# Kernel optimization log

Hardware: AMD Instinct MI355X
Metric: run time of the kernel (lower is better)

The kernel has to match this reference:

```python
import math
import jax, jax.numpy as jnp
import numpy as np

L, D, H, DFF, T, B, BUCKETS = 4, 512, 8, 2048, 256, 8, 32
DH = D // H


def _ln(x, g, b, eps=1e-6):
    m = x.mean(-1, keepdims=True)
    v = ((x - m) ** 2).mean(-1, keepdims=True)
    return (x - m) / jnp.sqrt(v + eps) * g + b


def setup_inputs() -> dict:
    key = jax.random.key(0)
    ki = iter(jax.random.split(key, 32))
    p = lambda shape: jax.random.normal(next(ki), shape, jnp.float32) * 0.02
    inp = {}
    inp['src'] = jax.random.normal(next(ki), (T, B, D), jnp.float32)
    inp['lengths'] = jax.random.randint(next(ki), (B,), 128, T + 1)
    inp['distances'] = jax.random.randint(next(ki), (B, T, T), 0, BUCKETS + 1)
    inp['u'] = jax.random.normal(next(ki), (D,), jnp.float32)
    inp['v'] = jax.random.normal(next(ki), (D,), jnp.float32)
    inp['ln1_g'] = jnp.ones((L, D)); inp['ln1_b'] = jnp.zeros((L, D))
    for nm in ['Wq', 'Wk', 'Wv', 'Wo']:
        inp[nm] = p((L, D, D))
    for nm in ['bq', 'bk', 'bv', 'bo']:
        inp[nm] = jnp.zeros((L, D))
    # learned relative-position embedding table per layer, padding row zeroed
    inp['rel_table'] = p((L, BUCKETS + 1, D)).at[:, BUCKETS, :].set(0.0)
    inp['ffn_ln_g'] = jnp.ones((L, D)); inp['ffn_ln_b'] = jnp.zeros((L, D))
    inp['W1'] = p((L, DFF, D)); inp['b1'] = jnp.zeros((L, DFF))
    inp['W2'] = p((L, D, DFF)); inp['b2'] = jnp.zeros((L, D))
    inp['final_ln_g'] = jnp.ones((D,)); inp['final_ln_b'] = jnp.zeros((D,))
    return inp


def reference(src, lengths, distances, u, v, ln1_g, ln1_b, Wq, bq, Wk, bk, Wv, bv,
              Wo, bo, rel_table, ffn_ln_g, ffn_ln_b, W1, b1, W2, b2,
              final_ln_g, final_ln_b):
    # onmt-style sinusoidal positional encoding with sqrt(d_model) scaling
    pos = jnp.arange(T, dtype=jnp.float32)[:, None]
    div = jnp.exp(jnp.arange(0, D, 2, dtype=jnp.float32) * (-math.log(10000.0) / D))
    pe = jnp.zeros((T, D)).at[:, 0::2].set(jnp.sin(pos * div)).at[:, 1::2].set(jnp.cos(pos * div))
    x = (src * math.sqrt(D) + pe[:, None, :]).transpose(1, 0, 2)  # (B,T,D)
    pad = jnp.arange(T)[None, :] >= lengths[:, None]  # (B,T), True = masked key
    uh = u.reshape(1, H, 1, DH)
    vh = v.reshape(1, H, 1, DH)
    for l in range(L):
        h = _ln(x, ln1_g[l], ln1_b[l])
        def heads(w, b_):
            return (h @ w.T + b_).reshape(B, T, H, DH).transpose(0, 2, 1, 3)
        q = heads(Wq[l], bq[l]) / math.sqrt(DH)  # (B,H,T,DH)
        k = heads(Wk[l], bk[l])
        val = heads(Wv[l], bv[l])
        # content term a_c = (q + u) k^T
        a_c = jnp.einsum('bhqd,bhkd->bhqk', q + uh, k)
        # relative term b_d = (q + v) R^T, R gathered per (query,key) pair
        rel = rel_table[l][distances].reshape(B, T, T, H, DH)  # (B,Q,K,H,DH)
        b_d = jnp.einsum('bhqd,bqkhd->bhqk', q + vh, rel)
        scores = (a_c + b_d).astype(jnp.float32)
        scores = jnp.where(pad[:, None, None, :], -1e18, scores)
        attn = jax.nn.softmax(scores, axis=-1)
        ctx = jnp.einsum('bhqk,bhkd->bhqd', attn, val)
        ctx = ctx.transpose(0, 2, 1, 3).reshape(B, T, D)
        out = ctx @ Wo[l].T + bo[l] + x  # residual (dropout=0)
        # PositionwiseFeedForward: LN -> W1 -> relu -> W2 -> +residual
        h2 = _ln(out, ffn_ln_g[l], ffn_ln_b[l])
        x = jax.nn.relu(h2 @ W1[l].T + b1[l]) @ W2[l].T + b2[l] + out
    x = _ln(x, final_ln_g, final_ln_b)
    return x.transpose(1, 0, 2)  # (T,B,D)
```

## Files before the change

kernel.cpp:

```cpp
#include <hip/hip_runtime.h>
#include <hip/hip_bf16.h>
#include <math.h>

constexpr int L = 4, D = 512, H = 8, DFF = 2048, T = 256, B = 8, BUCKETS = 32;
constexpr int DH = D / H;
constexpr int NT = B * T;
constexpr int QKVLD = 3 * D;

typedef __attribute__((ext_vector_type(8))) short bf16x8;
typedef __attribute__((ext_vector_type(4))) float f32x4;

__device__ __forceinline__ unsigned short f2bf(float f) {
    unsigned int x = __float_as_uint(f);
    return (unsigned short)((x + 0x7fffu + ((x >> 16) & 1u)) >> 16);
}
__device__ __forceinline__ float bf2f(unsigned short u) {
    return __uint_as_float((unsigned int)u << 16);
}

__device__ __forceinline__ void stage16(const unsigned short* g, short* l) {
    __builtin_amdgcn_global_load_lds((const __attribute__((address_space(1))) unsigned int*)g,
                                     (__attribute__((address_space(3))) unsigned int*)l,
                                     16, 0, 0);
}

__global__ __launch_bounds__(256) void embed_kernel(const float* __restrict__ src,
                                                    float* __restrict__ x)
{
    int idx = blockIdx.x * 256 + threadIdx.x;
    int d = idx & (D - 1);
    int t = (idx >> 9) & (T - 1);
    int b = idx >> 17;
    int i = d >> 1;
    float div = expf(-(float)(2 * i) * (9.210340371976184f / (float)D));
    float ang = (float)t * div;
    float pe = (d & 1) ? cosf(ang) : sinf(ang);
    x[idx] = src[((size_t)t * B + b) * D + d] * 22.62741699796952f + pe;
}

__device__ __forceinline__ void ln_core(const float* __restrict__ xr,
                                        const float* __restrict__ g,
                                        const float* __restrict__ bb,
                                        float* o0, float* o1, int tid)
{
    float v0 = xr[tid], v1 = xr[tid + 256];
    float s = v0 + v1, q2 = v0 * v0 + v1 * v1;
#pragma unroll
    for (int o = 32; o; o >>= 1) { s += __shfl_xor(s, o); q2 += __shfl_xor(q2, o); }
    __shared__ float rs[4], rq[4];
    int lane = tid & 63, wid = tid >> 6;
    if (lane == 0) { rs[wid] = s; rq[wid] = q2; }
    __syncthreads();
    s = rs[0] + rs[1] + rs[2] + rs[3];
    q2 = rq[0] + rq[1] + rq[2] + rq[3];
    float mean = s * (1.f / (float)D);
    float var = q2 * (1.f / (float)D) - mean * mean;
    float rstd = rsqrtf(var + 1e-6f);
    *o0 = (v0 - mean) * rstd * g[tid] + bb[tid];
    *o1 = (v1 - mean) * rstd * g[tid + 256] + bb[tid + 256];
}

__global__ __launch_bounds__(256) void ln_kernel(const float* __restrict__ x,
                                                 unsigned short* __restrict__ y,
                                                 const float* __restrict__ g,
                                                 const float* __restrict__ bb)
{
    int row = blockIdx.x, tid = threadIdx.x;
    float o0, o1;
    ln_core(x + (size_t)row * D, g, bb, &o0, &o1, tid);
    y[(size_t)row * D + tid] = f2bf(o0);
    y[(size_t)row * D + tid + 256] = f2bf(o1);
}

__global__ __launch_bounds__(256) void final_ln_kernel(const float* __restrict__ x,
                                                       float* __restrict__ out,
                                                       const float* __restrict__ g,
                                                       const float* __restrict__ bb)
{
    int row = blockIdx.x, tid = threadIdx.x;
    int b = row >> 8, t = row & (T - 1);
    float o0, o1;
    ln_core(x + (size_t)row * D, g, bb, &o0, &o1, tid);
    float* op = out + ((size_t)t * B + b) * D;
    op[tid] = o0;
    op[tid + 256] = o1;
}

__global__ __launch_bounds__(256) void convert_layer_kernel(
    const float* __restrict__ Wq, const float* __restrict__ Wk, const float* __restrict__ Wv,
    const float* __restrict__ Wo, const float* __restrict__ W1, const float* __restrict__ W2,
    const float* __restrict__ bq, const float* __restrict__ bk, const float* __restrict__ bv,
    const float* __restrict__ rel, int l,
    unsigned short* __restrict__ WQKVb, unsigned short* __restrict__ Wob,
    unsigned short* __restrict__ W1b, unsigned short* __restrict__ W2b,
    unsigned short* __restrict__ relb,
    float* __restrict__ bqkv)
{
    int g = blockIdx.x * 256 + threadIdx.x;
    const float* src; unsigned short* dst;
    bool zero = false;
    if (g < 98304) {
        int e = g * 8; int piece = e >> 18; int rem = e & 262143;
        src = (piece == 0 ? Wq : piece == 1 ? Wk : Wv) + (size_t)l * 262144 + rem;
        dst = WQKVb + e;
    } else if (g < 131072) {
        int e = (g - 98304) * 8;
        src = Wo + (size_t)l * 262144 + e; dst = Wob + e;
    } else if (g < 262144) {
        int e = (g - 131072) * 8;
        src = W1 + (size_t)l * 1048576 + e; dst = W1b + e;
    } else if (g < 393216) {
        int e = (g - 262144) * 8;
        src = W2 + (size_t)l * 1048576 + e; dst = W2b + e;
    } else {
        int e = (g - 393216) * 8;
        int row = e >> 9, cc = e & 511;
        dst = relb + e;
        if (row < BUCKETS + 1) src = rel + ((size_t)l * (BUCKETS + 1) + row) * 512 + cc;
        else { src = nullptr; zero = true; }
    }
    uint4 o;
    if (zero) { o.x = o.y = o.z = o.w = 0u; }
    else {
        float4 x = *(const float4*)src, y = *(const float4*)(src + 4);
        o.x = (unsigned)f2bf(x.x) | ((unsigned)f2bf(x.y) << 16);
        o.y = (unsigned)f2bf(x.z) | ((unsigned)f2bf(x.w) << 16);
        o.z = (unsigned)f2bf(y.x) | ((unsigned)f2bf(y.y) << 16);
        o.w = (unsigned)f2bf(y.z) | ((unsigned)f2bf(y.w) << 16);
    }
    *(uint4*)dst = o;
    if (g < 3 * D) {
        int piece = g >> 9, r2 = g & 511;
        bqkv[g] = (piece == 0 ? bq : piece == 1 ? bk : bv)[l * 512 + r2];
    }
}

template <bool RELU, bool RESID, bool OUTBF16>
__global__ __launch_bounds__(256) void mgemm_kernel(
    const unsigned short* __restrict__ A,
    const unsigned short* __restrict__ W,
    const float* __restrict__ bias,
    const float* __restrict__ resid,
    void* __restrict__ Cv,
    int N, int M, int K)
{
    __shared__ short smA[2][128 * 32];
    __shared__ short smB[2][128 * 32];
    int tid = threadIdx.x;
    int bn = blockIdx.y * 128;
    int bm = blockIdx.x * 128;
    const unsigned short* Ab = A + (size_t)bn * K;
    const unsigned short* Wb = W + (size_t)bm * K;

    f32x4 acc[4][4];
#pragma unroll
    for (int i = 0; i < 4; i++)
#pragma unroll
        for (int j = 0; j < 4; j++) acc[i][j] = (f32x4){0.f, 0.f, 0.f, 0.f};

    const int c0 = tid, c1 = tid + 256;
    const int r0 = c0 >> 2, p0 = c0 & 3, l0 = p0 ^ ((r0 >> 1) & 3);
    const int r1 = c1 >> 2, p1 = c1 & 3, l1 = p1 ^ ((r1 >> 1) & 3);

    auto stage = [&](int buf, int k0) {
        stage16(Ab + (size_t)r0 * K + k0 + l0 * 8, &smA[buf][c0 * 8]);
        stage16(Ab + (size_t)r1 * K + k0 + l1 * 8, &smA[buf][c1 * 8]);
        stage16(Wb + (size_t)r0 * K + k0 + l0 * 8, &smB[buf][c0 * 8]);
        stage16(Wb + (size_t)r1 * K + k0 + l1 * 8, &smB[buf][c1 * 8]);
    };

    const int lane = tid & 63;
    const int wv = tid >> 6, wr = wv >> 1, wc = wv & 1;
    int aoff[4], boff[4];
#pragma unroll
    for (int i = 0; i < 4; i++) {
        int ra = wr * 64 + i * 16 + (lane & 15);
        int ca = (lane >> 4) ^ ((ra >> 1) & 3);
        aoff[i] = ra * 32 + ca * 8;
        int rb = wc * 64 + i * 16 + (lane & 15);
        int cb = (lane >> 4) ^ ((rb >> 1) & 3);
        boff[i] = rb * 32 + cb * 8;
    }

    stage(0, 0);
    const int nkt = K >> 5;
    for (int kt = 0; kt < nkt; ++kt) {
        __syncthreads();
        int cur = kt & 1;
        if (kt + 1 < nkt) stage(cur ^ 1, (kt + 1) << 5);
        const short* sa = smA[cur];
        const short* sb = smB[cur];
        bf16x8 af[4], bfr[4];
#pragma unroll
        for (int i = 0; i < 4; i++) af[i] = *(const bf16x8*)(sa + aoff[i]);
#pragma unroll
        for (int j = 0; j < 4; j++) bfr[j] = *(const bf16x8*)(sb + boff[j]);
#pragma unroll
        for (int i = 0; i < 4; i++)
#pragma unroll
            for (int j = 0; j < 4; j++)
                acc[i][j] = __builtin_amdgcn_mfma_f32_16x16x32_bf16(af[i], bfr[j], acc[i][j], 0, 0, 0);
    }

#pragma unroll
    for (int j = 0; j < 4; j++) {
        int col = bm + wc * 64 + j * 16 + (lane & 15);
        float bval = bias[col];
#pragma unroll
        for (int i = 0; i < 4; i++) {
            f32x4 v = acc[i][j];
#pragma unroll
            for (int r = 0; r < 4; r++) {
                int row = bn + wr * 64 + i * 16 + (lane >> 4) * 4 + r;
                float val = v[r] + bval;
                if (RELU) val = fmaxf(val, 0.f);
                if (RESID) val += resid[(size_t)row * M + col];
                if (OUTBF16) ((unsigned short*)Cv)[(size_t)row * M + col] = f2bf(val);
                else         ((float*)Cv)[(size_t)row * M + col] = val;
            }
        }
    }
}

__global__ __launch_bounds__(256) void vtrans_kernel(const unsigned short* __restrict__ qkv,
                                                     unsigned short* __restrict__ vt)
{
    __shared__ unsigned short tile[64 * 66];
    int bh = blockIdx.x, b = bh >> 3, h = bh & 7;
    int kc = blockIdx.y * 64;
    int tid = threadIdx.x;
    int r = tid >> 2, c0 = (tid & 3) * 16;
    const unsigned short* rp = qkv + (size_t)(b * T + kc + r) * QKVLD + 2 * D + h * 64 + c0;
    uint4 w0 = *(const uint4*)rp;
    uint4 w1 = *(const uint4*)(rp + 8);
    unsigned short* tp = &tile[r * 66 + c0];
    unsigned int ww[8] = {w0.x, w0.y, w0.z, w0.w, w1.x, w1.y, w1.z, w1.w};
#pragma unroll
    for (int e = 0; e < 8; e++) {
        tp[2 * e]     = (unsigned short)(ww[e] & 0xffffu);
        tp[2 * e + 1] = (unsigned short)(ww[e] >> 16);
    }
    __syncthreads();
    int d = tid >> 2, k0 = (tid & 3) * 16;
    unsigned int outw[8];
#pragma unroll
    for (int i = 0; i < 8; i++) {
        unsigned int lo = tile[(k0 + 2 * i) * 66 + d];
        unsigned int hi = tile[(k0 + 2 * i + 1) * 66 + d];
        outw[i] = lo | (hi << 16);
    }
    unsigned short* op = vt + (size_t)(bh * 64 + d) * 256 + kc + k0;
    *(uint4*)op = *(uint4*)&outw[0];
    *(uint4*)(op + 8) = *(uint4*)&outw[4];
}

__global__ __launch_bounds__(256) void fattn_kernel(
    const unsigned short* __restrict__ qkv,
    const unsigned short* __restrict__ vt,
    const unsigned short* __restrict__ relb,
    const float* __restrict__ uvec,
    const float* __restrict__ vvec,
    const int* __restrict__ dist,
    const int* __restrict__ lengths,
    unsigned short* __restrict__ ctx)
{
    __shared__ unsigned short Ps[4][16][256];
    __shared__ float Qrel[4][16][49];

    int bh = blockIdx.x, b = bh >> 3, h = bh & 7;
    int qi0 = blockIdx.y * 64;
    int tid = threadIdx.x, w = tid >> 6, lane = tid & 63;
    int l15 = lane & 15, g = lane >> 4;
    int qr = qi0 + w * 16;

    const unsigned short* qbase = qkv + (size_t)(b * T + qr + l15) * QKVLD + h * 64 + g * 8;
    bf16x8 qa0 = *(const bf16x8*)(qbase);
    bf16x8 qa1 = *(const bf16x8*)(qbase + 32);

    bf16x8 qu0, qu1;
    {
        const float* up = uvec + h * 64 + g * 8;
        float ua0[8], ua1[8];
        *(float4*)&ua0[0] = *(const float4*)(up);
        *(float4*)&ua0[4] = *(const float4*)(up + 4);
        *(float4*)&ua1[0] = *(const float4*)(up + 32);
        *(float4*)&ua1[4] = *(const float4*)(up + 36);
#pragma unroll
        for (int e = 0; e < 8; e++) {
            qu0[e] = (short)f2bf(0.125f * bf2f((unsigned short)qa0[e]) + ua0[e]);
            qu1[e] = (short)f2bf(0.125f * bf2f((unsigned short)qa1[e]) + ua1[e]);
        }
    }

    {
        const float* vp = vvec + h * 64 + g * 8;
        float va0[8], va1[8];
        *(float4*)&va0[0] = *(const float4*)(vp);
        *(float4*)&va0[4] = *(const float4*)(vp + 4);
        *(float4*)&va1[0] = *(const float4*)(vp + 32);
        *(float4*)&va1[4] = *(const float4*)(vp + 36);
        bf16x8 qh0, qh1;
#pragma unroll
        for (int e = 0; e < 8; e++) {
            qh0[e] = (short)f2bf(0.125f * bf2f((unsigned short)qa0[e]) + va0[e]);
            qh1[e] = (short)f2bf(0.125f * bf2f((unsigned short)qa1[e]) + va1[e]);
        }
        f32x4 qacc[3];
#pragma unroll
        for (int j = 0; j < 3; j++) qacc[j] = (f32x4){0.f, 0.f, 0.f, 0.f};
#pragma unroll
        for (int j = 0; j < 3; j++) {
            const unsigned short* rp = relb + (size_t)(j * 16 + l15) * 512 + h * 64 + g * 8;
            bf16x8 r0 = *(const bf16x8*)(rp);
            bf16x8 r1 = *(const bf16x8*)(rp + 32);
            qacc[j] = __builtin_amdgcn_mfma_f32_16x16x32_bf16(qh0, r0, qacc[j], 0, 0, 0);
            qacc[j] = __builtin_amdgcn_mfma_f32_16x16x32_bf16(qh1, r1, qacc[j], 0, 0, 0);
        }
#pragma unroll
        for (int j = 0; j < 3; j++)
#pragma unroll
            for (int r = 0; r < 4; r++)
                Qrel[w][g * 4 + r][j * 16 + l15] = qacc[j][r];
    }

    f32x4 acc[16];
#pragma unroll
    for (int j = 0; j < 16; j++) acc[j] = (f32x4){0.f, 0.f, 0.f, 0.f};
    const unsigned short* kbase = qkv + (size_t)(b * T) * QKVLD + 512 + h * 64 + g * 8;
#pragma unroll
    for (int j = 0; j < 16; j++) {
        const unsigned short* kp = kbase + (size_t)(j * 16 + l15) * QKVLD;
        bf16x8 k0 = *(const bf16x8*)(kp);
        bf16x8 k1 = *(const bf16x8*)(kp + 32);
        acc[j] = __builtin_amdgcn_mfma_f32_16x16x32_bf16(qu0, k0, acc[j], 0, 0, 0);
        acc[j] = __builtin_amdgcn_mfma_f32_16x16x32_bf16(qu1, k1, acc[j], 0, 0, 0);
    }

    int len = lengths[b];
    float rinv[4];
    const int* db = dist + (size_t)b * T * T;
#pragma unroll
    for (int r = 0; r < 4; r++) {
        int rowloc = g * 4 + r;
        int qrow = qr + rowloc;
        const int* dpr = db + (size_t)qrow * T;
        float m = -3.0e38f;
#pragma unroll
        for (int j = 0; j < 16; j++) {
            int ki = j * 16 + l15;
            int dv = dpr[ki];
            float s = acc[j][r] + Qrel[w][rowloc][dv];
            s = (ki < len) ? s : -1.0e30f;
            acc[j][r] = s;
            m = fmaxf(m, s);
        }
#pragma unroll
        for (int o = 8; o; o >>= 1) m = fmaxf(m, __shfl_xor(m, o));
        float sum = 0.f;
#pragma unroll
        for (int j = 0; j < 16; j++) {
            int ki = j * 16 + l15;
            float p = __expf(acc[j][r] - m);
            sum += p;
            int cph = ((ki >> 3) ^ (rowloc & 7));
            Ps[w][rowloc][cph * 8 + (ki & 7)] = f2bf(p);
        }
#pragma unroll
        for (int o = 8; o; o >>= 1) sum += __shfl_xor(sum, o);
        rinv[r] = 1.0f / sum;
    }

    f32x4 oacc[4];
#pragma unroll
    for (int j = 0; j < 4; j++) oacc[j] = (f32x4){0.f, 0.f, 0.f, 0.f};
    const unsigned short* vtb = vt + (size_t)bh * 64 * 256;
#pragma unroll
    for (int ks = 0; ks < 8; ks++) {
        int c = ks * 4 + g;
        int cph = c ^ (l15 & 7);
        bf16x8 pa = *(const bf16x8*)&Ps[w][l15][cph * 8];
#pragma unroll
        for (int j2 = 0; j2 < 4; j2++) {
            bf16x8 vb = *(const bf16x8*)(vtb + (size_t)(j2 * 16 + l15) * 256 + c * 8);
            oacc[j2] = __builtin_amdgcn_mfma_f32_16x16x32_bf16(pa, vb, oacc[j2], 0, 0, 0);
        }
    }

#pragma unroll
    for (int j2 = 0; j2 < 4; j2++) {
#pragma unroll
        for (int r = 0; r < 4; r++) {
            int qrow = qr + g * 4 + r;
            int dcol = j2 * 16 + l15;
            ctx[(size_t)(b * T + qrow) * D + h * 64 + dcol] = f2bf(oacc[j2][r] * rinv[r]);
        }
    }
}

extern "C" void kernel_launch(void* const* d_in, const int* in_sizes, int n_in,
                              void* d_out, int out_size, void* d_ws, size_t ws_size,
                              hipStream_t stream)
{
    const float* src     = (const float*)d_in[0];
    const int*   lengths = (const int*)d_in[1];
    const int*   dist    = (const int*)d_in[2];
    const float* u       = (const float*)d_in[3];
    const float* v       = (const float*)d_in[4];
    const float* ln1_g   = (const float*)d_in[5];
    const float* ln1_b   = (const float*)d_in[6];
    const float* Wq      = (const float*)d_in[7];
    const float* Wk      = (const float*)d_in[8];
    const float* Wv      = (const float*)d_in[9];
    const float* Wo      = (const float*)d_in[10];
    const float* bq      = (const float*)d_in[11];
    const float* bk      = (const float*)d_in[12];
    const float* bv      = (const float*)d_in[13];
    const float* bo      = (const float*)d_in[14];
    const float* rel     = (const float*)d_in[15];
    const float* fg      = (const float*)d_in[16];
    const float* fb      = (const float*)d_in[17];
    const float* W1      = (const float*)d_in[18];
    const float* b1      = (const float*)d_in[19];
    const float* W2      = (const float*)d_in[20];
    const float* b2      = (const float*)d_in[21];
    const float* flg     = (const float*)d_in[22];
    const float* flb     = (const float*)d_in[23];

    float* ws = (float*)d_ws;
    float*          X     = ws;
    unsigned short* QKVb  = (unsigned short*)(ws + 1048576);
    unsigned short* Hb    = (unsigned short*)(ws + 2621440);
    unsigned short* CTX   = (unsigned short*)(ws + 3145728);
    unsigned short* FF1   = (unsigned short*)(ws + 3670016);
    unsigned short* VT    = (unsigned short*)(ws + 5767168);
    unsigned short* WQKVb = (unsigned short*)(ws + 6307840);
    unsigned short* Wob   = (unsigned short*)(ws + 6701056);
    unsigned short* W1b   = (unsigned short*)(ws + 6832128);
    unsigned short* W2b   = (unsigned short*)(ws + 7356416);
    float*          bqkv  = ws + 7880704;
    unsigned short* RELb  = (unsigned short*)(ws + 7882240);

    embed_kernel<<<4096, 256, 0, stream>>>(src, X);

    for (int l = 0; l < L; l++) {
        convert_layer_kernel<<<1548, 256, 0, stream>>>(
            Wq, Wk, Wv, Wo, W1, W2, bq, bk, bv, rel, l,
            WQKVb, Wob, W1b, W2b, RELb, bqkv);

        ln_kernel<<<NT, 256, 0, stream>>>(X, Hb, ln1_g + l * D, ln1_b + l * D);

        mgemm_kernel<false, false, true><<<dim3(12, 16), 256, 0, stream>>>(
            Hb, WQKVb, bqkv, nullptr, QKVb, NT, QKVLD, D);

        vtrans_kernel<<<dim3(64, 4), 256, 0, stream>>>(QKVb, VT);

        fattn_kernel<<<dim3(B * H, T / 64), 256, 0, stream>>>(
            QKVb, VT, RELb, u, v, dist, lengths, CTX);

        mgemm_kernel<false, true, false><<<dim3(4, 16), 256, 0, stream>>>(
            CTX, Wob, bo + l * D, X, X, NT, D, D);

        ln_kernel<<<NT, 256, 0, stream>>>(X, Hb, fg + l * D, fb + l * D);

        mgemm_kernel<true, false, true><<<dim3(16, 16), 256, 0, stream>>>(
            Hb, W1b, b1 + l * DFF, nullptr, FF1, NT, DFF, D);

        mgemm_kernel<false, true, false><<<dim3(4, 16), 256, 0, stream>>>(
            FF1, W2b, b2 + l * D, X, X, NT, D, DFF);
    }

    final_ln_kernel<<<NT, 256, 0, stream>>>(X, (float*)d_out, flg, flb);
}
```

Before: 617.1 us.

## Split-K the narrow output GEMMs and fuse partial reduction with residual LayerNorm

Measured after the change: 521.8 us. -15.4%, faster.

```diff
diff --git a/kernel.cpp b/kernel.cpp
--- a/kernel.cpp
+++ b/kernel.cpp
@@ -27,23 +27,30 @@
 __global__ __launch_bounds__(256) void embed_kernel(const float* __restrict__ src,
                                                     float* __restrict__ x)
 {
-    int idx = blockIdx.x * 256 + threadIdx.x;
-    int d = idx & (D - 1);
-    int t = (idx >> 9) & (T - 1);
-    int b = idx >> 17;
-    int i = d >> 1;
-    float div = expf(-(float)(2 * i) * (9.210340371976184f / (float)D));
-    float ang = (float)t * div;
-    float pe = (d & 1) ? cosf(ang) : sinf(ang);
-    x[idx] = src[((size_t)t * B + b) * D + d] * 22.62741699796952f + pe;
-}
-
-__device__ __forceinline__ void ln_core(const float* __restrict__ xr,
+    int t = blockIdx.x, tid = threadIdx.x;
+    float pe0, pe1;
+    {
+        int d0 = tid, d1 = tid + 256;
+        float dv0 = expf(-(float)(2 * (d0 >> 1)) * (9.210340371976184f / (float)D));
+        float dv1 = expf(-(float)(2 * (d1 >> 1)) * (9.210340371976184f / (float)D));
+        float a0 = (float)t * dv0, a1 = (float)t * dv1;
+        pe0 = (d0 & 1) ? cosf(a0) : sinf(a0);
+        pe1 = (d1 & 1) ? cosf(a1) : sinf(a1);
+    }
+#pragma unroll
+    for (int b = 0; b < B; b++) {
+        const float* sp = src + ((size_t)t * B + b) * D;
+        float* xp = x + ((size_t)(b * T + t)) * D;
+        xp[tid]       = sp[tid]       * 22.62741699796952f + pe0;
+        xp[tid + 256] = sp[tid + 256] * 22.62741699796952f + pe1;
+    }
+}
+
+__device__ __forceinline__ void ln_vals(float v0, float v1,
                                         const float* __restrict__ g,
                                         const float* __restrict__ bb,
                                         float* o0, float* o1, int tid)
 {
-    float v0 = xr[tid], v1 = xr[tid + 256];
     float s = v0 + v1, q2 = v0 * v0 + v1 * v1;
 #pragma unroll
     for (int o = 32; o; o >>= 1) { s += __shfl_xor(s, o); q2 += __shfl_xor(q2, o); }
@@ -66,56 +73,90 @@
                                                  const float* __restrict__ bb)
 {
     int row = blockIdx.x, tid = threadIdx.x;
+    float v0 = x[(size_t)row * D + tid], v1 = x[(size_t)row * D + tid + 256];
     float o0, o1;
-    ln_core(x + (size_t)row * D, g, bb, &o0, &o1, tid);
+    ln_vals(v0, v1, g, bb, &o0, &o1, tid);
     y[(size_t)row * D + tid] = f2bf(o0);
     y[(size_t)row * D + tid + 256] = f2bf(o1);
 }
 
-__global__ __launch_bounds__(256) void final_ln_kernel(const float* __restrict__ x,
-                                                       float* __restrict__ out,
-                                                       const float* __restrict__ g,
-                                                       const float* __restrict__ bb)
+__global__ __launch_bounds__(256) void lnr_kernel(float* __restrict__ X,
+                                                  const float* __restrict__ P,
+                                                  const float* __restrict__ bias,
+                                                  unsigned short* __restrict__ y,
+                                                  const float* __restrict__ g,
+                                                  const float* __restrict__ bb)
+{
+    int row = blockIdx.x, tid = threadIdx.x;
+    float v0 = X[(size_t)row * D + tid] + bias[tid];
+    float v1 = X[(size_t)row * D + tid + 256] + bias[tid + 256];
+#pragma unroll
+    for (int s = 0; s < 4; s++) {
+        v0 += P[((size_t)s * NT + row) * D + tid];
+        v1 += P[((size_t)s * NT + row) * D + tid + 256];
+    }
+    X[(size_t)row * D + tid] = v0;
+    X[(size_t)row * D + tid + 256] = v1;
+    float o0, o1;
+    ln_vals(v0, v1, g, bb, &o0, &o1, tid);
+    y[(size_t)row * D + tid] = f2bf(o0);
+    y[(size_t)row * D + tid + 256] = f2bf(o1);
+}
+
+__global__ __launch_bounds__(256) void final_lnr_kernel(const float* __restrict__ X,
+                                                        const float* __restrict__ P,
+                                                        const float* __restrict__ bias,
+                                                        float* __restrict__ out,
+                                                        const float* __restrict__ g,
+                                                        const float* __restrict__ bb)
 {
     int row = blockIdx.x, tid = threadIdx.x;
     int b = row >> 8, t = row & (T - 1);
+    float v0 = X[(size_t)row * D + tid] + bias[tid];
+    float v1 = X[(size_t)row * D + tid + 256] + bias[tid + 256];
+#pragma unroll
+    for (int s = 0; s < 4; s++) {
+        v0 += P[((size_t)s * NT + row) * D + tid];
+        v1 += P[((size_t)s * NT + row) * D + tid + 256];
+    }
     float o0, o1;
-    ln_core(x + (size_t)row * D, g, bb, &o0, &o1, tid);
+    ln_vals(v0, v1, g, bb, &o0, &o1, tid);
     float* op = out + ((size_t)t * B + b) * D;
     op[tid] = o0;
     op[tid + 256] = o1;
 }
 
-__global__ __launch_bounds__(256) void convert_layer_kernel(
+__global__ __launch_bounds__(256) void convert_all_kernel(
     const float* __restrict__ Wq, const float* __restrict__ Wk, const float* __restrict__ Wv,
     const float* __restrict__ Wo, const float* __restrict__ W1, const float* __restrict__ W2,
     const float* __restrict__ bq, const float* __restrict__ bk, const float* __restrict__ bv,
-    const float* __restrict__ rel, int l,
+    const float* __restrict__ rel,
     unsigned short* __restrict__ WQKVb, unsigned short* __restrict__ Wob,
     unsigned short* __restrict__ W1b, unsigned short* __restrict__ W2b,
     unsigned short* __restrict__ relb,
     float* __restrict__ bqkv)
 {
+    int l = blockIdx.y;
     int g = blockIdx.x * 256 + threadIdx.x;
     const float* src; unsigned short* dst;
     bool zero = false;
     if (g < 98304) {
         int e = g * 8; int piece = e >> 18; int rem = e & 262143;
         src = (piece == 0 ? Wq : piece == 1 ? Wk : Wv) + (size_t)l * 262144 + rem;
-        dst = WQKVb + e;
+        dst = WQKVb + (size_t)l * 786432 + e;
     } else if (g < 131072) {
         int e = (g - 98304) * 8;
-        src = Wo + (size_t)l * 262144 + e; dst = Wob + e;
+        src = Wo + (size_t)l * 262144 + e; dst = Wob + (size_t)l * 262144 + e;
     } else if (g < 262144) {
         int e = (g - 131072) * 8;
-        src = W1 + (size_t)l * 1048576 + e; dst = W1b + e;
+        src = W1 + (size_t)l * 1048576 + e; dst = W1b + (size_t)l * 1048576 + e;
     } else if (g < 393216) {
         int e = (g - 262144) * 8;
-        src = W2 + (size_t)l * 1048576 + e; dst = W2b + e;
+        src = W2 + (size_t)l * 1048576 + e; dst = W2b + (size_t)l * 1048576 + e;
     } else {
         int e = (g - 393216) * 8;
         int row = e >> 9, cc = e & 511;
-        dst = relb + e;
+        dst = relb + (size_t)l * 24576 + e;
         if (row < BUCKETS + 1) src = rel + ((size_t)l * (BUCKETS + 1) + row) * 512 + cc;
         else { src = nullptr; zero = true; }
     }
@@ -131,16 +172,15 @@
     *(uint4*)dst = o;
     if (g < 3 * D) {
         int piece = g >> 9, r2 = g & 511;
-        bqkv[g] = (piece == 0 ? bq : piece == 1 ? bk : bv)[l * 512 + r2];
-    }
-}
-
-template <bool RELU, bool RESID, bool OUTBF16>
+        bqkv[l * 1536 + g] = (piece == 0 ? bq : piece == 1 ? bk : bv)[l * 512 + r2];
+    }
+}
+
+template <bool RELU, bool OUTBF16>
 __global__ __launch_bounds__(256) void mgemm_kernel(
     const unsigned short* __restrict__ A,
     const unsigned short* __restrict__ W,
     const float* __restrict__ bias,
-    const float* __restrict__ resid,
     void* __restrict__ Cv,
     int N, int M, int K)
 {
@@ -214,9 +254,88 @@
                 int row = bn + wr * 64 + i * 16 + (lane >> 4) * 4 + r;
                 float val = v[r] + bval;
                 if (RELU) val = fmaxf(val, 0.f);
-                if (RESID) val += resid[(size_t)row * M + col];
                 if (OUTBF16) ((unsigned short*)Cv)[(size_t)row * M + col] = f2bf(val);
                 else         ((float*)Cv)[(size_t)row * M + col] = val;
+            }
+        }
+    }
+}
+
+__global__ __launch_bounds__(256) void mgemm_splitk_kernel(
+    const unsigned short* __restrict__ A,
+    const unsigned short* __restrict__ W,
+    float* __restrict__ P,
+    int N, int M, int K, int Ksub)
+{
+    __shared__ short smA[2][128 * 32];
+    __shared__ short smB[2][128 * 32];
+    int tid = threadIdx.x;
+    int s = blockIdx.z;
+    int bn = blockIdx.y * 128;
+    int bm = blockIdx.x * 128;
+    const unsigned short* Ab = A + (size_t)bn * K + s * Ksub;
+    const unsigned short* Wb = W + (size_t)bm * K + s * Ksub;
+
+    f32x4 acc[4][4];
+#pragma unroll
+    for (int i = 0; i < 4; i++)
+#pragma unroll
+        for (int j = 0; j < 4; j++) acc[i][j] = (f32x4){0.f, 0.f, 0.f, 0.f};
+
+    const int c0 = tid, c1 = tid + 256;
+    const int r0 = c0 >> 2, p0 = c0 & 3, l0 = p0 ^ ((r0 >> 1) & 3);
+    const int r1 = c1 >> 2, p1 = c1 & 3, l1 = p1 ^ ((r1 >> 1) & 3);
+
+    auto stage = [&](int buf, int k0) {
+        stage16(Ab + (size_t)r0 * K + k0 + l0 * 8, &smA[buf][c0 * 8]);
+        stage16(Ab + (size_t)r1 * K + k0 + l1 * 8, &smA[buf][c1 * 8]);
+        stage16(Wb + (size_t)r0 * K + k0 + l0 * 8, &smB[buf][c0 * 8]);
+        stage16(Wb + (size_t)r1 * K + k0 + l1 * 8, &smB[buf][c1 * 8]);
+    };
+
+    const int lane = tid & 63;
+    const int wv = tid >> 6, wr = wv >> 1, wc = wv & 1;
+    int aoff[4], boff[4];
+#pragma unroll
+    for (int i = 0; i < 4; i++) {
+        int ra = wr * 64 + i * 16 + (lane & 15);
+        int ca = (lane >> 4) ^ ((ra >> 1) & 3);
+        aoff[i] = ra * 32 + ca * 8;
+        int rb = wc * 64 + i * 16 + (lane & 15);
+        int cb = (lane >> 4) ^ ((rb >> 1) & 3);
+        boff[i] = rb * 32 + cb * 8;
+    }
+
+    stage(0, 0);
+    const int nkt = Ksub >> 5;
+    for (int kt = 0; kt < nkt; ++kt) {
+        __syncthreads();
+        int cur = kt & 1;
+        if (kt + 1 < nkt) stage(cur ^ 1, (kt + 1) << 5);
+        const short* sa = smA[cur];
+        const short* sb = smB[cur];
+        bf16x8 af[4], bfr[4];
+#pragma unroll
+        for (int i = 0; i < 4; i++) af[i] = *(const bf16x8*)(sa + aoff[i]);
+#pragma unroll
+        for (int j = 0; j < 4; j++) bfr[j] = *(const bf16x8*)(sb + boff[j]);
+#pragma unroll
+        for (int i = 0; i < 4; i++)
+#pragma unroll
+            for (int j = 0; j < 4; j++)
+                acc[i][j] = __builtin_amdgcn_mfma_f32_16x16x32_bf16(af[i], bfr[j], acc[i][j], 0, 0, 0);
+    }
+
+#pragma unroll
+    for (int j = 0; j < 4; j++) {
+        int col = bm + wc * 64 + j * 16 + (lane & 15);
+#pragma unroll
+        for (int i = 0; i < 4; i++) {
+            f32x4 v = acc[i][j];
+#pragma unroll
+            for (int r = 0; r < 4; r++) {
+                int row = bn + wr * 64 + i * 16 + (lane >> 4) * 4 + r;
+                P[((size_t)s * N + row) * M + col] = v[r];
             }
         }
     }
@@ -433,41 +552,55 @@
     unsigned short* CTX   = (unsigned short*)(ws + 3145728);
     unsigned short* FF1   = (unsigned short*)(ws + 3670016);
     unsigned short* VT    = (unsigned short*)(ws + 5767168);
-    unsigned short* WQKVb = (unsigned short*)(ws + 6307840);
-    unsigned short* Wob   = (unsigned short*)(ws + 6701056);
-    unsigned short* W1b   = (unsigned short*)(ws + 6832128);
-    unsigned short* W2b   = (unsigned short*)(ws + 7356416);
-    float*          bqkv  = ws + 7880704;
-    unsigned short* RELb  = (unsigned short*)(ws + 7882240);
-
-    embed_kernel<<<4096, 256, 0, stream>>>(src, X);
+    float*          Pbuf  = ws + 6291456;
+    unsigned short* WQKVb = (unsigned short*)(ws + 10485760);
+    unsigned short* Wob   = (unsigned short*)(ws + 12058624);
+    unsigned short* W1b   = (unsigned short*)(ws + 12582912);
+    unsigned short* W2b   = (unsigned short*)(ws + 14680064);
+    unsigned short* RELb  = (unsigned short*)(ws + 16777216);
+    float*          bqkv  = ws + 16826368;
+
+    embed_kernel<<<T, 256, 0, stream>>>(src, X);
+
+    convert_all_kernel<<<dim3(1548, L), 256, 0, stream>>>(
+        Wq, Wk, Wv, Wo, W1, W2, bq, bk, bv, rel,
+        WQKVb, Wob, W1b, W2b, RELb, bqkv);
 
     for (int l = 0; l < L; l++) {
-        convert_layer_kernel<<<1548, 256, 0, stream>>>(
-            Wq, Wk, Wv, Wo, W1, W2, bq, bk, bv, rel, l,
-            WQKVb, Wob, W1b, W2b, RELb, bqkv);
-
-        ln_kernel<<<NT, 256, 0, stream>>>(X, Hb, ln1_g + l * D, ln1_b + l * D);
-
-        mgemm_kernel<false, false, true><<<dim3(12, 16), 256, 0, stream>>>(
-            Hb, WQKVb, bqkv, nullptr, QKVb, NT, QKVLD, D);
+        const unsigned short* wqkv = WQKVb + (size_t)l * 786432;
+        const unsigned short* wob  = Wob   + (size_t)l * 262144;
+        const unsigned short* w1b  = W1b   + (size_t)l * 1048576;
+        const unsigned short* w2b  = W2b   + (size_t)l * 1048576;
+        const unsigned short* relb = RELb  + (size_t)l * 24576;
+        const float*          bql  = bqkv  + (size_t)l * 1536;
+
+        if (l == 0)
+            ln_kernel<<<NT, 256, 0, stream>>>(X, Hb, ln1_g, ln1_b);
+        else
+            lnr_kernel<<<NT, 256, 0, stream>>>(X, Pbuf, b2 + (size_t)(l - 1) * D,
+                                               Hb, ln1_g + l * D, ln1_b + l * D);
+
+        mgemm_kernel<false, true><<<dim3(12, 16), 256, 0, stream>>>(
+            Hb, wqkv, bql, QKVb, NT, QKVLD, D);
 
         vtrans_kernel<<<dim3(64, 4), 256, 0, stream>>>(QKVb, VT);
 
         fattn_kernel<<<dim3(B * H, T / 64), 256, 0, stream>>>(
-            QKVb, VT, RELb, u, v, dist, lengths, CTX);
-
-        mgemm_kernel<false, true, false><<<dim3(4, 16), 256, 0, stream>>>(
-            CTX, Wob, bo + l * D, X, X, NT, D, D);
-
-        ln_kernel<<<NT, 256, 0, stream>>>(X, Hb, fg + l * D, fb + l * D);
-
-        mgemm_kernel<true, false, true><<<dim3(16, 16), 256, 0, stream>>>(
-            Hb, W1b, b1 + l * DFF, nullptr, FF1, NT, DFF, D);
-
-        mgemm_kernel<false, true, false><<<dim3(4, 16), 256, 0, stream>>>(
-            FF1, W2b, b2 + l * D, X, X, NT, D, DFF);
-    }
-
-    final_ln_kernel<<<NT, 256, 0, stream>>>(X, (float*)d_out, flg, flb);
-}
+            QKVb, VT, relb, u, v, dist, lengths, CTX);
+
+        mgemm_splitk_kernel<<<dim3(4, 16, 4), 256, 0, stream>>>(
+            CTX, wob, Pbuf, NT, D, D, D / 4);
+
+        lnr_kernel<<<NT, 256, 0, stream>>>(X, Pbuf, bo + (size_t)l * D,
+                                           Hb, fg + l * D, fb + l * D);
+
+        mgemm_kernel<true, true><<<dim3(16, 16), 256, 0, stream>>>(
+            Hb, w1b, b1 + (size_t)l * DFF, FF1, NT, DFF, D);
+
+        mgemm_splitk_kernel<<<dim3(4, 16, 4), 256, 0, stream>>>(
+            FF1, w2b, Pbuf, NT, D, DFF, DFF / 4);
+    }
+
+    final_lnr_kernel<<<NT, 256, 0, stream>>>(X, Pbuf, b2 + (size_t)(L - 1) * D,
+                                             (float*)d_out, flg, flb);
+}
```
